# Kernel optimization log

Hardware: AMD Instinct MI355X
Metric: run time of the kernel (lower is better)

Reference implementation:

```python
import jax, jax.numpy as jnp
import numpy as np

D_MODEL = 1024
H = 16
D_K = D_MODEL // H


def setup_inputs() -> dict:
    key = jax.random.key(0)
    ks = jax.random.split(key, 12)
    B, S = 4, 2048
    scale = 1.0 / np.sqrt(D_MODEL)
    inp = {
        "q": jax.random.normal(ks[0], (B, S, D_MODEL), jnp.float32),
        "k": jax.random.normal(ks[1], (B, S, D_MODEL), jnp.float32),
        "v": jax.random.normal(ks[2], (B, S, D_MODEL), jnp.float32),
        "mask": jnp.ones((1, 1, S, S), dtype=bool),
        "Wq": jax.random.normal(ks[3], (D_MODEL, D_MODEL), jnp.float32) * scale,
        "bq": jax.random.normal(ks[4], (D_MODEL,), jnp.float32) * scale,
        "Wk": jax.random.normal(ks[5], (D_MODEL, D_MODEL), jnp.float32) * scale,
        "bk": jax.random.normal(ks[6], (D_MODEL,), jnp.float32) * scale,
        "Wv": jax.random.normal(ks[7], (D_MODEL, D_MODEL), jnp.float32) * scale,
        "bv": jax.random.normal(ks[8], (D_MODEL,), jnp.float32) * scale,
        "Wo": jax.random.normal(ks[9], (D_MODEL, D_MODEL), jnp.float32) * scale,
        "bo": jax.random.normal(ks[10], (D_MODEL,), jnp.float32) * scale,
    }
    return inp


def reference(q, k, v, mask, Wq, bq, Wk, bk, Wv, bv, Wo, bo):
    B, S, D = q.shape
    # QKV projections (torch Linear: x @ W.T + b), split into heads [B,H,S,d_k]
    Q = (q @ Wq.T + bq).reshape(B, S, H, D_K).transpose(0, 2, 1, 3)
    K = (k @ Wk.T + bk).reshape(B, S, H, D_K).transpose(0, 2, 1, 3)
    V = (v @ Wv.T + bv).reshape(B, S, H, D_K).transpose(0, 2, 1, 3)
    # scaled dot-product attention; NOTE: original's masked_fill result is
    # discarded (non-inplace), so the mask has no effect — faithfully ignored.
    scores = jnp.einsum("bhqd,bhkd->bhqk", Q, K) / jnp.sqrt(jnp.float32(D_K))
    attn = jax.nn.softmax(scores, axis=-1)  # dropout = identity (eval mode)
    x = jnp.einsum("bhqk,bhkd->bhqd", attn, V)
    x = x.transpose(0, 2, 1, 3).reshape(B, S, D)
    return x @ Wo.T + bo
```

## Files before the change

kernel.cpp:

```cpp
#include <hip/hip_runtime.h>
#include <stdint.h>

#define Bb 4
#define Ss 2048
#define Dd 1024
#define Hh 16
#define DKk 64
#define Mm (Bb * Ss)

typedef __attribute__((ext_vector_type(4))) float f32x4;
typedef __attribute__((ext_vector_type(16))) float f32x16;
typedef __attribute__((ext_vector_type(4))) float f4v;
typedef __attribute__((ext_vector_type(8))) unsigned short us8;
typedef __attribute__((ext_vector_type(4))) unsigned short us4;
typedef __attribute__((ext_vector_type(8))) __bf16 bf16x8;

__device__ __forceinline__ unsigned short bfbits(__bf16 x) {
  union { __bf16 b; unsigned short u; } v; v.b = x; return v.u;
}
__device__ __forceinline__ uint32_t packbf(float lo, float hi) {
  union { __bf16 b[2]; uint32_t u; } v;
  v.b[0] = (__bf16)lo; v.b[1] = (__bf16)hi;
  return v.u;
}
__device__ __forceinline__ void plswap(uint32_t& a, uint32_t& b) {
  asm("v_permlane32_swap_b32 %0, %1" : "+v"(a), "+v"(b));
}
__device__ __forceinline__ void gl16(const unsigned short* g, unsigned short* l) {
  __builtin_amdgcn_global_load_lds(
      (__attribute__((address_space(1))) void*)(g),
      (__attribute__((address_space(3))) void*)(l), 16, 0, 0);
}

__global__ __launch_bounds__(256)
void split_hilo(const float* __restrict__ x, unsigned short* __restrict__ hi,
                unsigned short* __restrict__ lo, int n4) {
  int i = blockIdx.x * 256 + threadIdx.x;
  if (i >= n4) return;
  f4v v = *(const f4v*)(x + (size_t)i * 4);
  us4 h, l;
#pragma unroll
  for (int j = 0; j < 4; ++j) {
    __bf16 hb = (__bf16)v[j];
    h[j] = bfbits(hb);
    l[j] = bfbits((__bf16)(v[j] - (float)hb));
  }
  *(us4*)(hi + (size_t)i * 4) = h;
  *(us4*)(lo + (size_t)i * 4) = l;
}

__global__ __launch_bounds__(256)
void cvt_bf16(const float* __restrict__ x, unsigned short* __restrict__ out, int n4) {
  int i = blockIdx.x * 256 + threadIdx.x;
  if (i >= n4) return;
  f4v v = *(const f4v*)(x + (size_t)i * 4);
  us4 h;
#pragma unroll
  for (int j = 0; j < 4; ++j) h[j] = bfbits((__bf16)v[j]);
  *(us4*)(out + (size_t)i * 4) = h;
}

__global__ __launch_bounds__(256)
void cvt3_bf16(const float* __restrict__ x0, unsigned short* __restrict__ o0,
               const float* __restrict__ x1, unsigned short* __restrict__ o1,
               const float* __restrict__ x2, unsigned short* __restrict__ o2,
               int n4) {
  int i = blockIdx.x * 256 + threadIdx.x;
  if (i >= n4) return;
  const float* x = (blockIdx.y == 0) ? x0 : (blockIdx.y == 1) ? x1 : x2;
  unsigned short* o = (blockIdx.y == 0) ? o0 : (blockIdx.y == 1) ? o1 : o2;
  f4v v = *(const f4v*)(x + (size_t)i * 4);
  us4 h;
#pragma unroll
  for (int j = 0; j < 4; ++j) h[j] = bfbits((__bf16)v[j]);
  *(us4*)(o + (size_t)i * 4) = h;
}

template <bool BSPLIT, bool OUT_BF16>
__global__ __launch_bounds__(256)
void gemm_bt(const unsigned short* __restrict__ A,
             const unsigned short* __restrict__ Bh, const unsigned short* __restrict__ Bl,
             const float* __restrict__ bias, void* __restrict__ outp,
             int Kdim, int Ndim, float scale) {
  __shared__ unsigned short Ath[128 * 64];
  __shared__ unsigned short Bth[128 * 64];
  __shared__ unsigned short Btl[BSPLIT ? 128 * 64 : 8];

  const int tid = threadIdx.x;
  const int wave = tid >> 6, lane = tid & 63, g = lane >> 4, ln = lane & 15;
  const int wr = wave >> 1, wc = wave & 1;
  int dd = blockIdx.x;
  int orig = (dd & 7) * 64 + (dd >> 3);
  const int bm = (orig >> 3) * 128;
  const int bn = (orig & 7) * 128;

  const int srow = lane >> 3;
  const int schunk = (lane & 7) ^ srow;

  f32x4 acc[4][4] = {};

  for (int k0 = 0; k0 < Kdim; k0 += 64) {
    __syncthreads();
#pragma unroll
    for (int ii = 0; ii < 4; ++ii) {
      const int rA = wave * 32 + ii * 8;
      gl16(&A [(size_t)(bm + rA + srow) * Kdim + k0 + schunk * 8], &Ath[rA * 64]);
      gl16(&Bh[(size_t)(bn + rA + srow) * Kdim + k0 + schunk * 8], &Bth[rA * 64]);
      if constexpr (BSPLIT) {
        gl16(&Bl[(size_t)(bn + rA + srow) * Kdim + k0 + schunk * 8], &Btl[rA * 64]);
      }
    }
    __syncthreads();

#pragma unroll
    for (int ko = 0; ko < 2; ++ko) {
      bf16x8 ah[4], bh[4], bl[4];
#pragma unroll
      for (int i = 0; i < 4; ++i) {
        const int ra = wr * 64 + i * 16 + ln;
        const int rb = wc * 64 + i * 16 + ln;
        ah[i] = *(const bf16x8*)&Ath[ra * 64 + ((ko * 4 + g) ^ (ra & 7)) * 8];
        bh[i] = *(const bf16x8*)&Bth[rb * 64 + ((ko * 4 + g) ^ (rb & 7)) * 8];
        if constexpr (BSPLIT) {
          bl[i] = *(const bf16x8*)&Btl[rb * 64 + ((ko * 4 + g) ^ (rb & 7)) * 8];
        }
      }
#pragma unroll
      for (int i = 0; i < 4; ++i)
#pragma unroll
        for (int j = 0; j < 4; ++j) {
          acc[i][j] = __builtin_amdgcn_mfma_f32_16x16x32_bf16(ah[i], bh[j], acc[i][j], 0, 0, 0);
          if constexpr (BSPLIT) {
            acc[i][j] = __builtin_amdgcn_mfma_f32_16x16x32_bf16(ah[i], bl[j], acc[i][j], 0, 0, 0);
          }
        }
    }
  }

  float bvals[4];
#pragma unroll
  for (int j = 0; j < 4; ++j) bvals[j] = bias[bn + wc * 64 + j * 16 + ln];

#pragma unroll
  for (int i = 0; i < 4; ++i) {
    int row0 = bm + wr * 64 + i * 16 + g * 4;
#pragma unroll
    for (int j = 0; j < 4; ++j) {
      int col = bn + wc * 64 + j * 16 + ln;
#pragma unroll
      for (int r = 0; r < 4; ++r) {
        float vv = (acc[i][j][r] + bvals[j]) * scale;
        if constexpr (OUT_BF16) {
          ((unsigned short*)outp)[(size_t)(row0 + r) * Ndim + col] = bfbits((__bf16)vv);
        } else {
          ((float*)outp)[(size_t)(row0 + r) * Ndim + col] = vv;
        }
      }
    }
  }
}

__global__ __launch_bounds__(256)
void transpose_v(const unsigned short* __restrict__ Vb, unsigned short* __restrict__ VT) {
  __shared__ unsigned short tb[64 * 72];
  int s0 = blockIdx.x * 64, d0 = blockIdx.y * 64, b = blockIdx.z;
  int tid = threadIdx.x;
#pragma unroll
  for (int chi = 0; chi < 2; ++chi) {
    int c = tid + chi * 256;
    int r = c >> 3, cc = (c & 7) * 8;
    *(us8*)&tb[r * 72 + cc] = *(const us8*)&Vb[((size_t)b * Ss + s0 + r) * Dd + d0 + cc];
  }
  __syncthreads();
#pragma unroll
  for (int chi = 0; chi < 2; ++chi) {
    int c = tid + chi * 256;
    int r = c >> 3, cc = (c & 7) * 8;
    us8 o;
#pragma unroll
    for (int j = 0; j < 8; ++j) o[j] = tb[(cc + j) * 72 + r];
    *(us8*)&VT[((size_t)b * Dd + d0 + r) * Ss + s0 + cc] = o;
  }
}

__global__ __launch_bounds__(256, 4)
void attn_fused(const unsigned short* __restrict__ Qb, const unsigned short* __restrict__ Kb,
                const unsigned short* __restrict__ VT, unsigned short* __restrict__ xb) {
  __shared__ unsigned short Ks[2][64 * 64];
  __shared__ unsigned short Vs[2][64 * 64];

  const int tid = threadIdx.x, wave = tid >> 6, lane = tid & 63;
  const int lq = lane & 31, hi = lane >> 5;
  const int swzc = (lane & 7) ^ ((lane >> 3) & 7);

  int dd = blockIdx.x;
  int orig = (dd & 7) * 128 + (dd >> 3);
  const int bh = orig >> 4, qb = orig & 15;
  const int q0 = qb * 128;
  const int b = bh >> 4, h = bh & 15;

  const size_t rowBase = (size_t)b * Ss * Dd + (size_t)h * DKk;
  const size_t vtBase  = ((size_t)b * Dd + h * DKk) * Ss;

  bf16x8 qf[4];
  {
    const unsigned short* qrow =
        Qb + rowBase + (size_t)(q0 + wave * 32 + lq) * Dd + 8 * hi;
#pragma unroll
    for (int c = 0; c < 4; ++c) qf[c] = *(const bf16x8*)(qrow + 16 * c);
  }

  bf16x8 ones;
#pragma unroll
  for (int j = 0; j < 8; ++j) ones[j] = (__bf16)1.0f;

  f32x16 accO[2] = {};
  f32x16 acc_l = {};

  const int i0 = wave * 2;
  auto stage = [&](int t, int nb) {
#pragma unroll
    for (int ii = 0; ii < 2; ++ii) {
      const int i = i0 + ii;
      const int rr = i * 8 + (lane >> 3);
      gl16(&Kb[rowBase + (size_t)(t * 64 + rr) * Dd + swzc * 8], &Ks[nb][i * 512]);
      gl16(&VT[vtBase + (size_t)rr * Ss + t * 64 + swzc * 8], &Vs[nb][i * 512]);
    }
  };

  stage(0, 0);

  for (int t = 0; t < 32; ++t) {
    const int cur = t & 1;
    __syncthreads();
    if (t + 1 < 32) stage(t + 1, 1 - cur);

    uint32_t pf[4][4];
#pragma unroll
    for (int s = 0; s < 2; ++s) {
      f32x16 z = {};
#pragma unroll
      for (int c = 0; c < 4; ++c) {
        bf16x8 kf = *(const bf16x8*)
            &Ks[cur][(s * 32 + lq) * 64 + ((2 * c + hi) ^ (lq & 7)) * 8];
        z = __builtin_amdgcn_mfma_f32_32x32x16_bf16(kf, qf[c], z, 0, 0, 0);
      }
      uint32_t w[8];
#pragma unroll
      for (int i = 0; i < 8; ++i) {
        float e0 = __builtin_amdgcn_exp2f(z[2 * i]);
        float e1 = __builtin_amdgcn_exp2f(z[2 * i + 1]);
        w[i] = packbf(e0, e1);
      }
#pragma unroll
      for (int mm = 0; mm < 2; ++mm) {
        uint32_t a0 = w[4 * mm + 0], b0 = w[4 * mm + 2];
        uint32_t a1 = w[4 * mm + 1], b1 = w[4 * mm + 3];
        plswap(a0, b0);
        plswap(a1, b1);
        pf[2 * s + mm][0] = a0;
        pf[2 * s + mm][1] = a1;
        pf[2 * s + mm][2] = b0;
        pf[2 * s + mm][3] = b1;
      }
    }

    __builtin_amdgcn_s_setprio(1);
#pragma unroll
    for (int m = 0; m < 4; ++m) {
      bf16x8 pa = *(const bf16x8*)&pf[m][0];
      acc_l = __builtin_amdgcn_mfma_f32_32x32x16_bf16(pa, ones, acc_l, 0, 0, 0);
#pragma unroll
      for (int ds = 0; ds < 2; ++ds) {
        bf16x8 bv = *(const bf16x8*)
            &Vs[cur][(ds * 32 + lq) * 64 + ((2 * m + hi) ^ (lq & 7)) * 8];
        accO[ds] = __builtin_amdgcn_mfma_f32_32x32x16_bf16(pa, bv, accO[ds], 0, 0, 0);
      }
    }
    __builtin_amdgcn_s_setprio(0);
  }

#pragma unroll
  for (int ds = 0; ds < 2; ++ds)
#pragma unroll
    for (int r = 0; r < 16; ++r) {
      int q = (r & 3) + 8 * (r >> 2) + 4 * hi;
      size_t row = (size_t)b * Ss + q0 + wave * 32 + q;
      xb[row * Dd + h * DKk + ds * 32 + lq] =
          bfbits((__bf16)(accO[ds][r] / acc_l[r]));
    }
}

extern "C" void kernel_launch(void* const* d_in, const int* in_sizes, int n_in,
                              void* d_out, int out_size, void* d_ws, size_t ws_size,
                              hipStream_t stream) {
  const float* q  = (const float*)d_in[0];
  const float* k  = (const float*)d_in[1];
  const float* v  = (const float*)d_in[2];
  const float* Wq = (const float*)d_in[4];
  const float* bq = (const float*)d_in[5];
  const float* Wk = (const float*)d_in[6];
  const float* bk = (const float*)d_in[7];
  const float* Wv = (const float*)d_in[8];
  const float* bv = (const float*)d_in[9];
  const float* Wo = (const float*)d_in[10];
  const float* bo = (const float*)d_in[11];

  char* ws = (char*)d_ws;
  const size_t SZT = (size_t)Mm * Dd * 2;
  const size_t SZW = (size_t)Dd * Dd * 2;
  const size_t need = 5 * SZT + 8 * SZW;
  if (ws_size < need) return;

  unsigned short* sh  = (unsigned short*)(ws);
  unsigned short* sl  = (unsigned short*)(ws + SZT);
  char* wbase = ws + 2 * SZT;
  unsigned short* Wqh = (unsigned short*)(wbase + 0 * SZW);
  unsigned short* Wkh = (unsigned short*)(wbase + 2 * SZW);
  unsigned short* Wvh = (unsigned short*)(wbase + 4 * SZW);
  unsigned short* Wvl = (unsigned short*)(wbase + 5 * SZW);
  unsigned short* Woh = (unsigned short*)(wbase + 6 * SZW);
  char* base2 = wbase + 8 * SZW;
  unsigned short* Qb = (unsigned short*)(base2 + 0 * SZT);
  unsigned short* Kb = (unsigned short*)(base2 + 1 * SZT);
  unsigned short* Vb = (unsigned short*)(base2 + 2 * SZT);
  unsigned short* VTp = sl;
  unsigned short* xbp = sh;

  const int n4t = Mm * Dd / 4;
  const int n4w = Dd * Dd / 4;
  const float QSCALE = 0.125f * 1.44269504f;

  cvt3_bf16<<<dim3(n4w / 256, 3), 256, 0, stream>>>(Wq, Wqh, Wk, Wkh, Wo, Woh, n4w);
  split_hilo<<<n4w / 256, 256, 0, stream>>>(Wv, Wvh, Wvl, n4w);

  cvt_bf16<<<n4t / 256, 256, 0, stream>>>(q, sh, n4t);
  gemm_bt<false, true><<<512, 256, 0, stream>>>(sh, Wqh, Wqh, bq, Qb, Dd, Dd, QSCALE);
  cvt_bf16<<<n4t / 256, 256, 0, stream>>>(k, sh, n4t);
  gemm_bt<false, true><<<512, 256, 0, stream>>>(sh, Wkh, Wkh, bk, Kb, Dd, Dd, 1.0f);
  cvt_bf16<<<n4t / 256, 256, 0, stream>>>(v, sh, n4t);
  gemm_bt<true, true><<<512, 256, 0, stream>>>(sh, Wvh, Wvl, bv, Vb, Dd, Dd, 1.0f);

  transpose_v<<<dim3(Ss / 64, Dd / 64, Bb), 256, 0, stream>>>(Vb, VTp);

  attn_fused<<<1024, 256, 0, stream>>>(Qb, Kb, VTp, xbp);

  gemm_bt<false, false><<<512, 256, 0, stream>>>(xbp, Woh, Woh, bo, d_out, Dd, Dd, 1.0f);
}
```

Before: 247.8 us.

## Fuse V transpose into V-projection GEMM epilogue and batch input conversions

Adds a dedicated V-projection GEMM that stages its bias-added bf16 output tile in shared memory and writes it out already transposed. This removes the separate transpose_v kernel and its extra round trip of V through global memory. The three separate activation-conversion launches are also merged into one cvt3_bf16 launch, which needs distinct workspace buffers for q, k and v instead of one reused buffer. The new epilogue costs extra shared-memory traffic and synchronisation inside the GEMM.

```diff
diff --git a/kernel.cpp b/kernel.cpp
--- a/kernel.cpp
+++ b/kernel.cpp
@@ -47,17 +47,6 @@
   }
   *(us4*)(hi + (size_t)i * 4) = h;
   *(us4*)(lo + (size_t)i * 4) = l;
-}
-
-__global__ __launch_bounds__(256)
-void cvt_bf16(const float* __restrict__ x, unsigned short* __restrict__ out, int n4) {
-  int i = blockIdx.x * 256 + threadIdx.x;
-  if (i >= n4) return;
-  f4v v = *(const f4v*)(x + (size_t)i * 4);
-  us4 h;
-#pragma unroll
-  for (int j = 0; j < 4; ++j) h[j] = bfbits((__bf16)v[j]);
-  *(us4*)(out + (size_t)i * 4) = h;
 }
 
 __global__ __launch_bounds__(256)
@@ -161,25 +150,86 @@
 }
 
 __global__ __launch_bounds__(256)
-void transpose_v(const unsigned short* __restrict__ Vb, unsigned short* __restrict__ VT) {
-  __shared__ unsigned short tb[64 * 72];
-  int s0 = blockIdx.x * 64, d0 = blockIdx.y * 64, b = blockIdx.z;
-  int tid = threadIdx.x;
-#pragma unroll
-  for (int chi = 0; chi < 2; ++chi) {
-    int c = tid + chi * 256;
-    int r = c >> 3, cc = (c & 7) * 8;
-    *(us8*)&tb[r * 72 + cc] = *(const us8*)&Vb[((size_t)b * Ss + s0 + r) * Dd + d0 + cc];
-  }
+void gemm_vT(const unsigned short* __restrict__ A,
+             const unsigned short* __restrict__ Bh, const unsigned short* __restrict__ Bl,
+             const float* __restrict__ bias, unsigned short* __restrict__ VT,
+             int Kdim, int Ndim) {
+  __shared__ unsigned short S[3 * 128 * 64];
+  unsigned short* Ath = S;
+  unsigned short* Bth = S + 8192;
+  unsigned short* Btl = S + 16384;
+
+  const int tid = threadIdx.x;
+  const int wave = tid >> 6, lane = tid & 63, g = lane >> 4, ln = lane & 15;
+  const int wr = wave >> 1, wc = wave & 1;
+  int dd = blockIdx.x;
+  int orig = (dd & 7) * 64 + (dd >> 3);
+  const int bm = (orig >> 3) * 128;
+  const int bn = (orig & 7) * 128;
+
+  const int srow = lane >> 3;
+  const int schunk = (lane & 7) ^ srow;
+
+  f32x4 acc[4][4] = {};
+
+  for (int k0 = 0; k0 < Kdim; k0 += 64) {
+    __syncthreads();
+#pragma unroll
+    for (int ii = 0; ii < 4; ++ii) {
+      const int rA = wave * 32 + ii * 8;
+      gl16(&A [(size_t)(bm + rA + srow) * Kdim + k0 + schunk * 8], &Ath[rA * 64]);
+      gl16(&Bh[(size_t)(bn + rA + srow) * Kdim + k0 + schunk * 8], &Bth[rA * 64]);
+      gl16(&Bl[(size_t)(bn + rA + srow) * Kdim + k0 + schunk * 8], &Btl[rA * 64]);
+    }
+    __syncthreads();
+
+#pragma unroll
+    for (int ko = 0; ko < 2; ++ko) {
+      bf16x8 ah[4], bh[4], bl[4];
+#pragma unroll
+      for (int i = 0; i < 4; ++i) {
+        const int ra = wr * 64 + i * 16 + ln;
+        const int rb = wc * 64 + i * 16 + ln;
+        ah[i] = *(const bf16x8*)&Ath[ra * 64 + ((ko * 4 + g) ^ (ra & 7)) * 8];
+        bh[i] = *(const bf16x8*)&Bth[rb * 64 + ((ko * 4 + g) ^ (rb & 7)) * 8];
+        bl[i] = *(const bf16x8*)&Btl[rb * 64 + ((ko * 4 + g) ^ (rb & 7)) * 8];
+      }
+#pragma unroll
+      for (int i = 0; i < 4; ++i)
+#pragma unroll
+        for (int j = 0; j < 4; ++j) {
+          acc[i][j] = __builtin_amdgcn_mfma_f32_16x16x32_bf16(ah[i], bh[j], acc[i][j], 0, 0, 0);
+          acc[i][j] = __builtin_amdgcn_mfma_f32_16x16x32_bf16(ah[i], bl[j], acc[i][j], 0, 0, 0);
+        }
+    }
+  }
+
+  float bvals[4];
+#pragma unroll
+  for (int j = 0; j < 4; ++j) bvals[j] = bias[bn + wc * 64 + j * 16 + ln];
+
   __syncthreads();
 #pragma unroll
-  for (int chi = 0; chi < 2; ++chi) {
-    int c = tid + chi * 256;
-    int r = c >> 3, cc = (c & 7) * 8;
-    us8 o;
-#pragma unroll
-    for (int j = 0; j < 8; ++j) o[j] = tb[(cc + j) * 72 + r];
-    *(us8*)&VT[((size_t)b * Dd + d0 + r) * Ss + s0 + cc] = o;
+  for (int i = 0; i < 4; ++i) {
+    int sl0 = wr * 64 + i * 16 + g * 4;
+#pragma unroll
+    for (int j = 0; j < 4; ++j) {
+      int dl = wc * 64 + j * 16 + ln;
+      us4 w;
+#pragma unroll
+      for (int r = 0; r < 4; ++r) w[r] = bfbits((__bf16)(acc[i][j][r] + bvals[j]));
+      *(us4*)&S[dl * 132 + sl0] = w;
+    }
+  }
+  __syncthreads();
+
+  const int bb = bm >> 11, s0g = bm & 2047;
+#pragma unroll
+  for (int it = 0; it < 8; ++it) {
+    int u = it * 256 + tid;
+    int dl = u >> 4, sc = (u & 15) * 8;
+    us8 o = *(const us8*)&S[dl * 132 + sc];
+    *(us8*)&VT[((size_t)bb * Dd + bn + dl) * Ss + s0g + sc] = o;
   }
 }
 
@@ -312,20 +362,20 @@
   const size_t need = 5 * SZT + 8 * SZW;
   if (ws_size < need) return;
 
-  unsigned short* sh  = (unsigned short*)(ws);
-  unsigned short* sl  = (unsigned short*)(ws + SZT);
-  char* wbase = ws + 2 * SZT;
+  unsigned short* ab_q = (unsigned short*)(ws + 0 * SZT);
+  unsigned short* ab_k = (unsigned short*)(ws + 1 * SZT);
+  unsigned short* ab_v = (unsigned short*)(ws + 2 * SZT);
+  char* wbase = ws + 3 * SZT;
   unsigned short* Wqh = (unsigned short*)(wbase + 0 * SZW);
-  unsigned short* Wkh = (unsigned short*)(wbase + 2 * SZW);
-  unsigned short* Wvh = (unsigned short*)(wbase + 4 * SZW);
-  unsigned short* Wvl = (unsigned short*)(wbase + 5 * SZW);
-  unsigned short* Woh = (unsigned short*)(wbase + 6 * SZW);
+  unsigned short* Wkh = (unsigned short*)(wbase + 1 * SZW);
+  unsigned short* Wvh = (unsigned short*)(wbase + 2 * SZW);
+  unsigned short* Wvl = (unsigned short*)(wbase + 3 * SZW);
+  unsigned short* Woh = (unsigned short*)(wbase + 4 * SZW);
   char* base2 = wbase + 8 * SZW;
   unsigned short* Qb = (unsigned short*)(base2 + 0 * SZT);
   unsigned short* Kb = (unsigned short*)(base2 + 1 * SZT);
-  unsigned short* Vb = (unsigned short*)(base2 + 2 * SZT);
-  unsigned short* VTp = sl;
-  unsigned short* xbp = sh;
+  unsigned short* VTp = ab_q;
+  unsigned short* xbp = ab_k;
 
   const int n4t = Mm * Dd / 4;
   const int n4w = Dd * Dd / 4;
@@ -334,14 +384,11 @@
   cvt3_bf16<<<dim3(n4w / 256, 3), 256, 0, stream>>>(Wq, Wqh, Wk, Wkh, Wo, Woh, n4w);
   split_hilo<<<n4w / 256, 256, 0, stream>>>(Wv, Wvh, Wvl, n4w);
 
-  cvt_bf16<<<n4t / 256, 256, 0, stream>>>(q, sh, n4t);
-  gemm_bt<false, true><<<512, 256, 0, stream>>>(sh, Wqh, Wqh, bq, Qb, Dd, Dd, QSCALE);
-  cvt_bf16<<<n4t / 256, 256, 0, stream>>>(k, sh, n4t);
-  gemm_bt<false, true><<<512, 256, 0, stream>>>(sh, Wkh, Wkh, bk, Kb, Dd, Dd, 1.0f);
-  cvt_bf16<<<n4t / 256, 256, 0, stream>>>(v, sh, n4t);
-  gemm_bt<true, true><<<512, 256, 0, stream>>>(sh, Wvh, Wvl, bv, Vb, Dd, Dd, 1.0f);
-
-  transpose_v<<<dim3(Ss / 64, Dd / 64, Bb), 256, 0, stream>>>(Vb, VTp);
+  cvt3_bf16<<<dim3(n4t / 256, 3), 256, 0, stream>>>(q, ab_q, k, ab_k, v, ab_v, n4t);
+
+  gemm_bt<false, true><<<512, 256, 0, stream>>>(ab_q, Wqh, Wqh, bq, Qb, Dd, Dd, QSCALE);
+  gemm_bt<false, true><<<512, 256, 0, stream>>>(ab_k, Wkh, Wkh, bk, Kb, Dd, Dd, 1.0f);
+  gemm_vT<<<512, 256, 0, stream>>>(ab_v, Wvh, Wvl, bv, VTp, Dd, Dd);
 
   attn_fused<<<1024, 256, 0, stream>>>(Qb, Kb, VTp, xbp);
 
```

Measured after the change: 237.0 us. 1.05x faster.
